# Kernel tuning notes

Measured on AMD Instinct MI355X. Metric: run time of the kernel, lower is better.

The kernel has to match this reference:

```python
import jax, jax.numpy as jnp
import numpy as np
import math

IMG = 224
PATCH = 14
E = 1024          # transformer width (ViT-L/14)
H = 16            # num heads
DH = E // H       # head dim
LAYERS = 24
FF = 4 * E        # CLIP MLP hidden
NROI = 32         # number of ROI bboxes
NSIDE = IMG // PATCH
NPATCH = NSIDE * NSIDE  # 256
T = 1 + NPATCH    # sequence length incl. CLS
INIT = 0.02
EPS_LN = 1e-5


def setup_inputs() -> dict:
    key = jax.random.key(0)
    ks = jax.random.split(key, 16)
    frame = jax.random.uniform(ks[0], (3, IMG, IMG), dtype=jnp.float32)
    # valid bboxes in pixel coords: x1<x2, y1<y2
    c = jax.random.uniform(ks[1], (NROI, 2), dtype=jnp.float32) * (IMG - 40.0) + 20.0
    s = jax.random.uniform(ks[2], (NROI, 2), dtype=jnp.float32) * 60.0 + 20.0
    bboxes = jnp.stack([c[:, 0] - s[:, 0] / 2, c[:, 1] - s[:, 1] / 2,
                        c[:, 0] + s[:, 0] / 2, c[:, 1] + s[:, 1] / 2], axis=-1)
    bboxes = jnp.clip(bboxes, 0.0, float(IMG))
    f32 = jnp.float32
    conv_w = jax.random.normal(ks[3], (E, 3, PATCH, PATCH), f32) * INIT
    cls_emb = jax.random.normal(ks[4], (E,), f32) * INIT
    wq = jax.random.normal(ks[5], (LAYERS, E, E), f32) * INIT
    wk = jax.random.normal(ks[6], (LAYERS, E, E), f32) * INIT
    wv = jax.random.normal(ks[7], (LAYERS, E, E), f32) * INIT
    wo = jax.random.normal(ks[8], (LAYERS, E, E), f32) * INIT
    bq = jnp.zeros((LAYERS, E), f32); bk = jnp.zeros((LAYERS, E), f32)
    bv = jnp.zeros((LAYERS, E), f32); bo = jnp.zeros((LAYERS, E), f32)
    ln1_s = jnp.ones((LAYERS, E), f32); ln1_b = jnp.zeros((LAYERS, E), f32)
    ln2_s = jnp.ones((LAYERS, E), f32); ln2_b = jnp.zeros((LAYERS, E), f32)
    w1 = jax.random.normal(ks[9], (LAYERS, E, FF), f32) * INIT
    b1 = jnp.zeros((LAYERS, FF), f32)
    w2 = jax.random.normal(ks[10], (LAYERS, FF, E), f32) * INIT
    b2 = jnp.zeros((LAYERS, E), f32)
    return {"frame": frame, "bboxes": bboxes, "conv_w": conv_w, "cls_emb": cls_emb,
            "ln1_s": ln1_s, "ln1_b": ln1_b, "wq": wq, "bq": bq, "wk": wk, "bk": bk,
            "wv": wv, "bv": bv, "wo": wo, "bo": bo, "ln2_s": ln2_s, "ln2_b": ln2_b,
            "w1": w1, "b1": b1, "w2": w2, "b2": b2}


def _patch_coords():
    r = jnp.arange(NSIDE, dtype=jnp.float32)
    c = jnp.arange(NSIDE, dtype=jnp.float32)
    cc, rr = jnp.meshgrid(c, r)  # row-major like the python loop
    x1 = (cc * PATCH).reshape(-1); y1 = (rr * PATCH).reshape(-1)
    return jnp.stack([x1, y1, x1 + PATCH, y1 + PATCH], axis=-1)  # (NPATCH,4)


def _overlap_ratio(bboxes, patches):
    # intersection area / patch area -> Mi (N, NPATCH)
    bx1, by1, bx2, by2 = [bboxes[:, None, i] for i in range(4)]
    px1, py1, px2, py2 = [patches[None, :, i] for i in range(4)]
    iw = jnp.clip(jnp.minimum(bx2, px2) - jnp.maximum(bx1, px1), 0.0)
    ih = jnp.clip(jnp.minimum(by2, py2) - jnp.maximum(by1, py1), 0.0)
    parea = (px2 - px1) * (py2 - py1)
    return iw * ih / parea


def _ln(x, s, b):
    m = jnp.mean(x, axis=-1, keepdims=True)
    v = jnp.var(x, axis=-1, keepdims=True)
    return (x - m) * jax.lax.rsqrt(v + EPS_LN) * s + b


def _quick_gelu(x):
    return x * jax.nn.sigmoid(1.702 * x)


def _forward(frame, bboxes, conv_w, cls_emb, ln1_s, ln1_b, wq, bq, wk, bk,
             wv, bv, wo, bo, ln2_s, ln2_b, w1, b1, w2, b2):
    # patch embed: conv stride=PATCH, then relu (as in module forward)
    x = jax.lax.conv_general_dilated(frame[None], conv_w, (PATCH, PATCH), 'VALID',
                                     dimension_numbers=('NCHW', 'OIHW', 'NCHW'))
    x = jax.nn.relu(x)                      # (1, E, NSIDE, NSIDE)
    x = x.reshape(E, NPATCH).T              # (NPATCH, E)
    x = jnp.concatenate([cls_emb[None, :], x], axis=0)  # (T, E)

    Mi = _overlap_ratio(bboxes, _patch_coords())  # (NROI, NPATCH)
    pb = Mi.sum(axis=0)
    pb = pb / (pb.max() + 1e-6)
    attn_bias = jnp.zeros((T, T), jnp.float32).at[0, 1:].set(pb)

    scale = 1.0 / math.sqrt(DH)

    def blk(x, p):
        l1s, l1b, Wq, Bq, Wk, Bk, Wv, Bv, Wo, Bo, l2s, l2b, W1, B1, W2, B2 = p
        h = _ln(x, l1s, l1b)
        q = (h @ Wq + Bq).reshape(T, H, DH)
        k = (h @ Wk + Bk).reshape(T, H, DH)
        v = (h @ Wv + Bv).reshape(T, H, DH)
        scores = jnp.einsum('lhd,shd->hls', q, k) * scale + attn_bias[None]
        a = jax.nn.softmax(scores, axis=-1)
        o = jnp.einsum('hls,shd->lhd', a, v).reshape(T, E) @ Wo + Bo
        x = x + o
        h2 = _ln(x, l2s, l2b)
        m = _quick_gelu(h2 @ W1 + B1) @ W2 + B2
        return x + m, None

    x, _ = jax.lax.scan(blk, x, (ln1_s, ln1_b, wq, bq, wk, bk, wv, bv, wo, bo,
                                 ln2_s, ln2_b, w1, b1, w2, b2))

    cls_out = x[0:1]            # (1, E)
    patch_out = x[1:]           # (NPATCH, E)
    roi = Mi @ patch_out        # (NROI, E)
    return jnp.concatenate([cls_out, roi], axis=0)  # (1+NROI, E)


def reference(frame, bboxes, conv_w, cls_emb, ln1_s, ln1_b, wq, bq, wk, bk,
              wv, bv, wo, bo, ln2_s, ln2_b, w1, b1, w2, b2):
    return _forward(frame, bboxes, conv_w, cls_emb, ln1_s, ln1_b, wq, bq, wk, bk,
                    wv, bv, wo, bo, ln2_s, ln2_b, w1, b1, w2, b2)
```

## Files before the change

kernel.cpp:

```cpp
#include <hip/hip_runtime.h>
#include <hip/hip_bf16.h>
#include <math.h>

#define E_DIM 1024
#define FF_DIM 4096
#define LAYERS 24
#define MPAD 384
#define SPAD 288
#define KCP 608

typedef __attribute__((ext_vector_type(8))) short short8;
typedef __attribute__((ext_vector_type(8))) __bf16 bf16x8;
typedef __attribute__((ext_vector_type(4))) float float4_t;
typedef __attribute__((ext_vector_type(4))) unsigned short ushort4_t;

union ABu { short8 s; bf16x8 b; };
union BFU { __bf16 b; unsigned short u; };

__device__ __forceinline__ float4_t MFMA(bf16x8 a, bf16x8 b, float4_t c) {
  return __builtin_amdgcn_mfma_f32_16x16x32_bf16(a, b, c, 0, 0, 0);
}
__device__ __forceinline__ float4_t MFMAs(short8 a, short8 b, float4_t c) {
  ABu ua, ub; ua.s = a; ub.s = b;
  return __builtin_amdgcn_mfma_f32_16x16x32_bf16(ua.b, ub.b, c, 0, 0, 0);
}
__device__ __forceinline__ unsigned short f2bf(float f) {
  BFU x; x.b = (__bf16)f; return x.u;
}

__device__ __forceinline__ void glds16(const float* src, float* dst) {
  __builtin_amdgcn_global_load_lds(
      (const __attribute__((address_space(1))) unsigned int*)src,
      (__attribute__((address_space(3))) unsigned int*)dst, 16, 0, 0);
}

__global__ void prep_kernel(const float* __restrict__ frame, const float* __restrict__ conv_w,
                            unsigned short* __restrict__ Pm, unsigned short* __restrict__ Wp,
                            unsigned short* __restrict__ h, unsigned short* __restrict__ ob,
                            unsigned short* __restrict__ vTb) {
  int b = blockIdx.x, tid = threadIdx.x;
  if (b < 256) {
    int pr = b >> 4, pc = b & 15;
    for (int kk = tid; kk < KCP; kk += 256) {
      unsigned short us = 0;
      if (kk < 588) {
        int c = kk / 196, rem = kk % 196;
        int i = rem / 14, j = rem % 14;
        us = f2bf(frame[c * 224 * 224 + (pr * 14 + i) * 224 + (pc * 14 + j)]);
      }
      Pm[b * KCP + kk] = us;
    }
  } else if (b < 1280) {
    int n = b - 256;
    for (int kk = tid; kk < KCP; kk += 256) {
      unsigned short us = (kk < 588) ? f2bf(conv_w[n * 588 + kk]) : (unsigned short)0;
      Wp[n * KCP + kk] = us;
    }
  } else {
    int idx = (b - 1280) * 256 + tid;
    const int NH = (MPAD - 257) * E_DIM;
    const int NO = (MPAD - 272) * E_DIM;
    const int NV = 16 * 64 * (SPAD - 272);
    if (idx < NH) {
      h[257 * E_DIM + idx] = 0;
    } else if (idx < NH + NO) {
      ob[272 * E_DIM + (idx - NH)] = 0;
    } else if (idx < NH + NO + NV) {
      int i = idx - NH - NO;
      vTb[(size_t)(i >> 4) * SPAD + 272 + (i & 15)] = 0;
    }
  }
}

__global__ void pb_cls_kernel(const float* __restrict__ bboxes, const float* __restrict__ cls_emb,
                              float* __restrict__ pb, float* __restrict__ Mi, float* __restrict__ x) {
  __shared__ float sb[128];
  __shared__ float red[256];
  int tid = threadIdx.x;
  if (tid < 128) sb[tid] = bboxes[tid];
  __syncthreads();
  int p = tid;
  float px1 = (float)((p & 15) * 14), py1 = (float)((p >> 4) * 14);
  float px2 = px1 + 14.f, py2 = py1 + 14.f;
  float s = 0.f;
  for (int r = 0; r < 32; ++r) {
    float bx1 = sb[r * 4 + 0], by1 = sb[r * 4 + 1], bx2 = sb[r * 4 + 2], by2 = sb[r * 4 + 3];
    float iw = fmaxf(fminf(bx2, px2) - fmaxf(bx1, px1), 0.f);
    float ih = fmaxf(fminf(by2, py2) - fmaxf(by1, py1), 0.f);
    float ov = iw * ih * (1.f / 196.f);
    Mi[r * 256 + p] = ov;
    s += ov;
  }
  red[tid] = s;
  __syncthreads();
  for (int off = 128; off > 0; off >>= 1) {
    if (tid < off) red[tid] = fmaxf(red[tid], red[tid + off]);
    __syncthreads();
  }
  pb[p] = s / (red[0] + 1e-6f);
  for (int j = 0; j < 4; ++j) x[tid * 4 + j] = cls_emb[tid * 4 + j];
}

__global__ __launch_bounds__(256) void conv_gemm(const unsigned short* __restrict__ Pm,
                                                 const unsigned short* __restrict__ Wp,
                                                 float* __restrict__ x) {
  int n0 = blockIdx.x * 16;
  int tid = threadIdx.x, wave = tid >> 6, lane = tid & 63;
  int lg = lane >> 4, lc = lane & 15;
  float4_t acc[4] = {{0,0,0,0},{0,0,0,0},{0,0,0,0},{0,0,0,0}};
  const unsigned short* bp = Wp + (size_t)(n0 + lc) * KCP + lg * 8;
  const unsigned short* apt[4];
#pragma unroll
  for (int t = 0; t < 4; ++t) apt[t] = Pm + (size_t)((wave + t * 4) * 16 + lc) * KCP + lg * 8;
  for (int s = 0; s < 19; ++s) {
    short8 bf = *(const short8*)bp; bp += 32;
#pragma unroll
    for (int t = 0; t < 4; ++t) {
      short8 af = *(const short8*)apt[t]; apt[t] += 32;
      acc[t] = MFMAs(af, bf, acc[t]);
    }
  }
#pragma unroll
  for (int t = 0; t < 4; ++t) {
    int mbase = (wave + t * 4) * 16 + lg * 4;
#pragma unroll
    for (int r = 0; r < 4; ++r)
      x[(size_t)(1 + mbase + r) * E_DIM + n0 + lc] = fmaxf(acc[t][r], 0.f);
  }
}

template <int NTOT, int EPI, int NK>
__global__ __launch_bounds__(256, 1) void gemm_nk(
    const unsigned short* __restrict__ A, int lda,
    const float* __restrict__ Wa, const float* __restrict__ Wb2, const float* __restrict__ Wc,
    const float* __restrict__ ba, const float* __restrict__ bb, const float* __restrict__ bc,
    int NNT,
    unsigned short* __restrict__ oq, unsigned short* __restrict__ okk,
    unsigned short* __restrict__ ovT, unsigned short* __restrict__ om,
    float* __restrict__ opart) {
  static_assert(NK >= 2, "pipeline needs >=2 K-tiles");
  __shared__ __align__(16) float Wt[3][128][32];
  int b = blockIdx.x;
  int p = ((b >> 4) << 3) | (b & 7);
  int mh = (b >> 3) & 1;
  int nt = p % NNT, ks = p / NNT;

  int tid = threadIdx.x, wave = tid >> 6, lane = tid & 63;
  int lg = lane >> 4, lc = lane & 15;

  const float* W; const float* bias; int ncl;
  if (EPI == 0) {
    int sel = nt >> 5; ncl = (nt & 31) << 5;
    W = (sel == 0) ? Wa : ((sel == 1) ? Wb2 : Wc);
    bias = (sel == 0) ? ba : ((sel == 1) ? bb : bc);
  } else {
    ncl = nt << 5; W = Wa; bias = ba;
  }

  const int kb0 = ks * (NK * 128);

  const float* wsrc[4];
  int dsto[4];
#pragma unroll
  for (int op = 0; op < 4; ++op) {
    int rbase = wave * 32 + op * 8;
    int row = rbase + (lane >> 3);
    int key = 8 * ((wave * 4 + op) & 3);
    int col = ((lane & 7) * 4) ^ key;
    wsrc[op] = W + (size_t)(kb0 + row) * NTOT + ncl + col;
    dsto[op] = __builtin_amdgcn_readfirstlane(rbase * 32);
  }

  const unsigned short* ap[3];
#pragma unroll
  for (int j = 0; j < 3; ++j) {
    int t0 = mh * 12 + wave * 3 + j;
    ap[j] = A + (size_t)(t0 * 16 + lc) * lda + kb0 + lg * 8;
  }

  float4_t acc[6];
#pragma unroll
  for (int i = 0; i < 6; ++i) acc[i] = (float4_t){0, 0, 0, 0};

  short8 av[2][12];
#pragma unroll
  for (int s = 0; s < 4; ++s)
#pragma unroll
    for (int j = 0; j < 3; ++j)
      av[0][s * 3 + j] = *(const short8*)(ap[j] + s * 32);
#pragma unroll
  for (int j = 0; j < 3; ++j) ap[j] += 128;

#pragma unroll
  for (int op = 0; op < 4; ++op) glds16(wsrc[op], &Wt[0][0][0] + dsto[op]);
#pragma unroll
  for (int op = 0; op < 4; ++op)
    glds16(wsrc[op] + (size_t)128 * NTOT, &Wt[1][0][0] + dsto[op]);
  asm volatile("s_waitcnt vmcnt(4)\n\ts_barrier" ::: "memory");

  const int cx0 = lg * 256 + (lc ^ (8 * lg));
  const int cx1 = lg * 256 + ((16 + lc) ^ (8 * lg));

#pragma unroll
  for (int t = 0; t < NK; ++t) {
    if (t + 1 < NK) {
#pragma unroll
      for (int s = 0; s < 4; ++s)
#pragma unroll
        for (int j = 0; j < 3; ++j)
          av[(t + 1) & 1][s * 3 + j] = *(const short8*)(ap[j] + s * 32);
#pragma unroll
      for (int j = 0; j < 3; ++j) ap[j] += 128;
    }
    if (t + 2 < NK) {
      float* bufn = &Wt[(t + 2) % 3][0][0];
#pragma unroll
      for (int op = 0; op < 4; ++op)
        glds16(wsrc[op] + (size_t)(t + 2) * 128 * NTOT, bufn + dsto[op]);
    }
    const float* Wb_ = &Wt[t % 3][0][0];
#pragma unroll
    for (int s = 0; s < 4; ++s) {
      bf16x8 wf0, wf1;
#pragma unroll
      for (int d = 0; d < 8; ++d) {
        wf0[d] = (__bf16)Wb_[s * 1024 + cx0 + d * 32];
        wf1[d] = (__bf16)Wb_[s * 1024 + cx1 + d * 32];
      }
#pragma unroll
      for (int j = 0; j < 3; ++j) {
        ABu a; a.s = av[t & 1][s * 3 + j];
        acc[j * 2 + 0] = MFMA(wf0, a.b, acc[j * 2 + 0]);
        acc[j * 2 + 1] = MFMA(wf1, a.b, acc[j * 2 + 1]);
      }
    }
    if (t + 1 < NK) {
      if (t + 2 < NK) asm volatile("s_waitcnt vmcnt(4)\n\ts_barrier" ::: "memory");
      else            asm volatile("s_waitcnt vmcnt(0)\n\ts_barrier" ::: "memory");
    }
  }

  float4_t bv0 = {0,0,0,0}, bv1 = {0,0,0,0};
  if (bias) {
    bv0 = *(const float4_t*)(bias + ncl + lg * 4);
    bv1 = *(const float4_t*)(bias + ncl + 16 + lg * 4);
  }

  if (EPI == 0) {
    int sel = nt >> 5;
    int head = ncl >> 6;
    int db0 = (ncl & 63) + lg * 4;
    int db1 = (ncl & 63) + 16 + lg * 4;
#pragma unroll
    for (int j = 0; j < 3; ++j) {
      int tile = mh * 12 + wave * 3 + j;
      int m = tile * 16 + lc;
      if (sel < 2) {
        unsigned short* dst = (sel == 0 ? oq : okk) + ((size_t)(head * MPAD + m)) * 64;
        ushort4_t h0, h1;
#pragma unroll
        for (int r = 0; r < 4; ++r) {
          h0[r] = f2bf(acc[j * 2 + 0][r] + bv0[r]);
          h1[r] = f2bf(acc[j * 2 + 1][r] + bv1[r]);
        }
        *(ushort4_t*)(dst + db0) = h0;
        *(ushort4_t*)(dst + db1) = h1;
      } else if (tile < 17) {
#pragma unroll
        for (int r = 0; r < 4; ++r) {
          ovT[(size_t)(head * 64 + db0 + r) * SPAD + m] = f2bf(acc[j * 2 + 0][r] + bv0[r]);
          ovT[(size_t)(head * 64 + db1 + r) * SPAD + m] = f2bf(acc[j * 2 + 1][r] + bv1[r]);
        }
      }
    }
  } else if (EPI == 1) {
#pragma unroll
    for (int j = 0; j < 3; ++j) {
      int m = (mh * 12 + wave * 3 + j) * 16 + lc;
      ushort4_t h0, h1;
#pragma unroll
      for (int r = 0; r < 4; ++r) {
        float v0 = acc[j * 2 + 0][r] + bv0[r];
        float v1 = acc[j * 2 + 1][r] + bv1[r];
        h0[r] = f2bf(v0 / (1.f + __expf(-1.702f * v0)));
        h1[r] = f2bf(v1 / (1.f + __expf(-1.702f * v1)));
      }
      *(ushort4_t*)(om + (size_t)m * FF_DIM + ncl + lg * 4) = h0;
      *(ushort4_t*)(om + (size_t)m * FF_DIM + ncl + 16 + lg * 4) = h1;
    }
  } else {
#pragma unroll
    for (int j = 0; j < 3; ++j) {
      int m = (mh * 12 + wave * 3 + j) * 16 + lc;
      float* dst = opart + ((size_t)ks * MPAD + m) * E_DIM + ncl + lg * 4;
      *(float4_t*)dst = acc[j * 2 + 0];
      *(float4_t*)(dst + 16) = acc[j * 2 + 1];
    }
  }
}

__global__ __launch_bounds__(256) void attn_kernel(
    const unsigned short* __restrict__ qb, const unsigned short* __restrict__ kb,
    const unsigned short* __restrict__ vT, const float* __restrict__ pb,
    unsigned short* __restrict__ ob) {
  int head = blockIdx.x / 17, qt = blockIdx.x % 17;
  int q0 = qt * 16;
  int tid = threadIdx.x, wave = tid >> 6, lane = tid & 63;
  int lg = lane >> 4, lc = lane & 15;
  const unsigned short* qh = qb + (size_t)head * MPAD * 64;
  const unsigned short* kh = kb + (size_t)head * MPAD * 64;
  const unsigned short* vh = vT + (size_t)head * 64 * SPAD;

  short8 aq0 = *(const short8*)(qh + (size_t)(q0 + lc) * 64 + lg * 8);
  short8 aq1 = *(const short8*)(qh + (size_t)(q0 + lc) * 64 + 32 + lg * 8);

  float4_t sc[5];
  int st[5]; int nst = 0;
#pragma unroll
  for (int j = 0; j < 5; ++j) {
    int t = wave + j * 4;
    st[j] = (t < 17) ? t : 0;
    if (t < 17) nst = j + 1;
    sc[j] = (float4_t){0,0,0,0};
  }
#pragma unroll
  for (int j = 0; j < 5; ++j) {
    if (j < nst) {
      const unsigned short* kp = kh + (size_t)(st[j] * 16 + lc) * 64 + lg * 8;
      short8 b0 = *(const short8*)kp;
      short8 b1 = *(const short8*)(kp + 32);
      sc[j] = MFMAs(aq0, b0, sc[j]);
      sc[j] = MFMAs(aq1, b1, sc[j]);
    }
  }
  float mx[4] = {-1e30f, -1e30f, -1e30f, -1e30f};
#pragma unroll
  for (int j = 0; j < 5; ++j) {
    if (j < nst) {
      int sg = st[j] * 16 + lc;
#pragma unroll
      for (int r = 0; r < 4; ++r) {
        float v = sc[j][r] * 0.125f;
        if (sg >= 257) v = -1e30f;
        else if (q0 + lg * 4 + r == 0 && sg >= 1) v += pb[sg - 1];
        sc[j][r] = v;
        mx[r] = fmaxf(mx[r], v);
      }
    }
  }
#pragma unroll
  for (int r = 0; r < 4; ++r) {
    mx[r] = fmaxf(mx[r], __shfl_xor(mx[r], 1, 64));
    mx[r] = fmaxf(mx[r], __shfl_xor(mx[r], 2, 64));
    mx[r] = fmaxf(mx[r], __shfl_xor(mx[r], 4, 64));
    mx[r] = fmaxf(mx[r], __shfl_xor(mx[r], 8, 64));
  }
  __shared__ float smax[4][16];
  __shared__ float sden[4][16];
  __shared__ __align__(16) unsigned short P[16][SPAD];
  if (lc == 0) {
#pragma unroll
    for (int r = 0; r < 4; ++r) smax[wave][lg * 4 + r] = mx[r];
  }
  __syncthreads();
  float fm[4], den[4] = {0, 0, 0, 0};
#pragma unroll
  for (int r = 0; r < 4; ++r) {
    int qq = lg * 4 + r;
    fm[r] = fmaxf(fmaxf(smax[0][qq], smax[1][qq]), fmaxf(smax[2][qq], smax[3][qq]));
  }
#pragma unroll
  for (int j = 0; j < 5; ++j) {
    if (j < nst) {
#pragma unroll
      for (int r = 0; r < 4; ++r) {
        float pe = __expf(sc[j][r] - fm[r]);
        sc[j][r] = pe;
        den[r] += pe;
      }
    }
  }
#pragma unroll
  for (int r = 0; r < 4; ++r) {
    den[r] += __shfl_xor(den[r], 1, 64);
    den[r] += __shfl_xor(den[r], 2, 64);
    den[r] += __shfl_xor(den[r], 4, 64);
    den[r] += __shfl_xor(den[r], 8, 64);
  }
  if (lc == 0) {
#pragma unroll
    for (int r = 0; r < 4; ++r) sden[wave][lg * 4 + r] = den[r];
  }
  P[tid >> 4][272 + (tid & 15)] = 0;
#pragma unroll
  for (int j = 0; j < 5; ++j) {
    if (j < nst) {
#pragma unroll
      for (int r = 0; r < 4; ++r) P[lg * 4 + r][st[j] * 16 + lc] = f2bf(sc[j][r]);
    }
  }
  __syncthreads();
  float denf[4];
#pragma unroll
  for (int r = 0; r < 4; ++r) {
    int qq = lg * 4 + r;
    denf[r] = sden[0][qq] + sden[1][qq] + sden[2][qq] + sden[3][qq];
  }
  int d0 = wave * 16;
  float4_t oa = {0, 0, 0, 0};
#pragma unroll
  for (int s9 = 0; s9 < 9; ++s9) {
    short8 pa = *(const short8*)(&P[lc][s9 * 32 + lg * 8]);
    short8 bv = *(const short8*)(vh + (size_t)(d0 + lc) * SPAD + s9 * 32 + lg * 8);
    oa = MFMAs(pa, bv, oa);
  }
#pragma unroll
  for (int r = 0; r < 4; ++r) {
    int qg = q0 + lg * 4 + r;
    ob[(size_t)qg * E_DIM + head * 64 + d0 + lc] = f2bf(oa[r] / denf[r]);
  }
}

__global__ __launch_bounds__(256) void reduce_ln_kernel(
    float* __restrict__ x, const float* __restrict__ part, int nparts,
    const float* __restrict__ rbias,
    const float* __restrict__ lns, const float* __restrict__ lnb,
    unsigned short* __restrict__ hout) {
  int m = blockIdx.x, tid = threadIdx.x;
  int c0 = tid * 4;
  float4_t v = *(const float4_t*)(x + (size_t)m * E_DIM + c0);
  if (rbias) v += *(const float4_t*)(rbias + c0);
  for (int s = 0; s < nparts; ++s)
    v += *(const float4_t*)(part + ((size_t)s * MPAD + m) * E_DIM + c0);
  if (nparts > 0) *(float4_t*)(x + (size_t)m * E_DIM + c0) = v;
  float s1 = v[0] + v[1] + v[2] + v[3];
  float s2 = v[0] * v[0] + v[1] * v[1] + v[2] * v[2] + v[3] * v[3];
#pragma unroll
  for (int off = 1; off < 64; off <<= 1) {
    s1 += __shfl_xor(s1, off, 64);
    s2 += __shfl_xor(s2, off, 64);
  }
  __shared__ float red[8];
  int wave = tid >> 6, lane = tid & 63;
  if (lane == 0) { red[wave * 2] = s1; red[wave * 2 + 1] = s2; }
  __syncthreads();
  s1 = red[0] + red[2] + red[4] + red[6];
  s2 = red[1] + red[3] + red[5] + red[7];
  float mean = s1 * (1.f / 1024.f);
  float var = s2 * (1.f / 1024.f) - mean * mean;
  float rstd = rsqrtf(var + 1e-5f);
  float4_t ls = *(const float4_t*)(lns + c0);
  float4_t lb = *(const float4_t*)(lnb + c0);
  ushort4_t hv;
#pragma unroll
  for (int r = 0; r < 4; ++r) hv[r] = f2bf((v[r] - mean) * rstd * ls[r] + lb[r]);
  *(ushort4_t*)(hout + (size_t)m * E_DIM + c0) = hv;
}

__global__ __launch_bounds__(256) void roi_kernel(const float* __restrict__ x,
                                                  const float* __restrict__ Mi,
                                                  float* __restrict__ out) {
  int b = blockIdx.x, tid = threadIdx.x;
  int c0 = tid * 4;
  if (b == 0) {
    *(float4_t*)(out + c0) = *(const float4_t*)(x + c0);
  } else {
    __shared__ float mi[256];
    mi[tid] = Mi[(b - 1) * 256 + tid];
    __syncthreads();
    float4_t acc = {0, 0, 0, 0};
    for (int p = 0; p < 256; ++p) {
      float4_t xv = *(const float4_t*)(x + (size_t)(1 + p) * E_DIM + c0);
      acc += mi[p] * xv;
    }
    *(float4_t*)(out + (size_t)b * E_DIM + c0) = acc;
  }
}

extern "C" void kernel_launch(void* const* d_in, const int* in_sizes, int n_in,
                              void* d_out, int out_size, void* d_ws, size_t ws_size,
                              hipStream_t stream) {
  const float* frame   = (const float*)d_in[0];
  const float* bboxes  = (const float*)d_in[1];
  const float* conv_w  = (const float*)d_in[2];
  const float* cls_emb = (const float*)d_in[3];
  const float* ln1_s   = (const float*)d_in[4];
  const float* ln1_b   = (const float*)d_in[5];
  const float* wq = (const float*)d_in[6];
  const float* bq = (const float*)d_in[7];
  const float* wk = (const float*)d_in[8];
  const float* bk = (const float*)d_in[9];
  const float* wv = (const float*)d_in[10];
  const float* bv = (const float*)d_in[11];
  const float* wo = (const float*)d_in[12];
  const float* bo = (const float*)d_in[13];
  const float* ln2_s = (const float*)d_in[14];
  const float* ln2_b = (const float*)d_in[15];
  const float* w1 = (const float*)d_in[16];
  const float* b1 = (const float*)d_in[17];
  const float* w2 = (const float*)d_in[18];
  const float* b2 = (const float*)d_in[19];

  char* base = (char*)d_ws;
  auto carve = [&](size_t bytes) {
    char* r = base;
    base += (bytes + 255) & ~(size_t)255;
    return r;
  };
  float* x            = (float*)carve((size_t)257 * E_DIM * 4);
  unsigned short* h   = (unsigned short*)carve((size_t)MPAD * E_DIM * 2);
  unsigned short* qb  = (unsigned short*)carve((size_t)16 * MPAD * 64 * 2);
  unsigned short* kbf = (unsigned short*)carve((size_t)16 * MPAD * 64 * 2);
  unsigned short* vTb = (unsigned short*)carve((size_t)16 * 64 * SPAD * 2);
  unsigned short* ob  = (unsigned short*)carve((size_t)MPAD * E_DIM * 2);
  unsigned short* mb  = (unsigned short*)carve((size_t)MPAD * FF_DIM * 2);
  float* part         = (float*)carve((size_t)4 * MPAD * E_DIM * 4);
  float* pbv          = (float*)carve(256 * 4);
  float* Mi           = (float*)carve(32 * 256 * 4);
  unsigned short* Pm  = (unsigned short*)carve((size_t)256 * KCP * 2);
  unsigned short* Wp  = (unsigned short*)carve((size_t)1024 * KCP * 2);

  prep_kernel<<<1280 + 1020, 256, 0, stream>>>(frame, conv_w, Pm, Wp, h, ob, vTb);
  pb_cls_kernel<<<1, 256, 0, stream>>>(bboxes, cls_emb, pbv, Mi, x);
  conv_gemm<<<64, 256, 0, stream>>>(Pm, Wp, x);
  reduce_ln_kernel<<<257, 256, 0, stream>>>(x, nullptr, 0, nullptr, ln1_s, ln1_b, h);

  for (int l = 0; l < LAYERS; ++l) {
    size_t o2  = (size_t)l * E_DIM * E_DIM;
    size_t o1  = (size_t)l * E_DIM;
    size_t of1 = (size_t)l * E_DIM * FF_DIM;
    size_t ofb = (size_t)l * FF_DIM;
    gemm_nk<1024, 0, 8><<<192, 256, 0, stream>>>(h, E_DIM, wq + o2, wk + o2, wv + o2,
                                                 bq + o1, bk + o1, bv + o1,
                                                 96, qb, kbf, vTb, nullptr, nullptr);
    attn_kernel<<<272, 256, 0, stream>>>(qb, kbf, vTb, pbv, ob);
    gemm_nk<1024, 2, 2><<<256, 256, 0, stream>>>(ob, E_DIM, wo + o2, nullptr, nullptr,
                                                 nullptr, nullptr, nullptr,
                                                 32, nullptr, nullptr, nullptr, nullptr, part);
    reduce_ln_kernel<<<257, 256, 0, stream>>>(x, part, 4, bo + o1, ln2_s + o1, ln2_b + o1, h);
    gemm_nk<4096, 1, 8><<<256, 256, 0, stream>>>(h, E_DIM, w1 + of1, nullptr, nullptr,
                                                 b1 + ofb, nullptr, nullptr,
                                                 128, nullptr, nullptr, nullptr, mb, nullptr);
    gemm_nk<1024, 2, 8><<<256, 256, 0, stream>>>(mb, FF_DIM, w2 + of1, nullptr, nullptr,
                                                 nullptr, nullptr, nullptr,
                                                 32, nullptr, nullptr, nullptr, nullptr, part);
    const float* nls = (l < LAYERS - 1) ? (ln1_s + (size_t)(l + 1) * E_DIM) : ln1_s;
    const float* nlb = (l < LAYERS - 1) ? (ln1_b + (size_t)(l + 1) * E_DIM) : ln1_b;
    reduce_ln_kernel<<<257, 256, 0, stream>>>(x, part, 4, b2 + o1, nls, nlb, h);
  }
  roi_kernel<<<33, 256, 0, stream>>>(x, Mi, (float*)d_out);
}
```

Baseline: 2.042 ms.

## Stage GEMM weights through registers as bf16 in LDS with manual pipeline

After: 1.800 ms. 1.13x faster.

```diff
diff --git a/kernel.cpp b/kernel.cpp
--- a/kernel.cpp
+++ b/kernel.cpp
@@ -17,21 +17,12 @@
 union ABu { short8 s; bf16x8 b; };
 union BFU { __bf16 b; unsigned short u; };
 
-__device__ __forceinline__ float4_t MFMA(bf16x8 a, bf16x8 b, float4_t c) {
-  return __builtin_amdgcn_mfma_f32_16x16x32_bf16(a, b, c, 0, 0, 0);
-}
 __device__ __forceinline__ float4_t MFMAs(short8 a, short8 b, float4_t c) {
   ABu ua, ub; ua.s = a; ub.s = b;
   return __builtin_amdgcn_mfma_f32_16x16x32_bf16(ua.b, ub.b, c, 0, 0, 0);
 }
 __device__ __forceinline__ unsigned short f2bf(float f) {
   BFU x; x.b = (__bf16)f; return x.u;
-}
-
-__device__ __forceinline__ void glds16(const float* src, float* dst) {
-  __builtin_amdgcn_global_load_lds(
-      (const __attribute__((address_space(1))) unsigned int*)src,
-      (__attribute__((address_space(3))) unsigned int*)dst, 16, 0, 0);
 }
 
 __global__ void prep_kernel(const float* __restrict__ frame, const float* __restrict__ conv_w,
@@ -129,6 +120,9 @@
   }
 }
 
+#define WAITB(n) asm volatile("s_waitcnt vmcnt(" #n ") lgkmcnt(0)\n\ts_barrier" ::: "memory")
+#define WAITV(n) asm volatile("s_waitcnt vmcnt(" #n ")" ::: "memory")
+
 template <int NTOT, int EPI, int NK>
 __global__ __launch_bounds__(256, 1) void gemm_nk(
     const unsigned short* __restrict__ A, int lda,
@@ -138,8 +132,8 @@
     unsigned short* __restrict__ oq, unsigned short* __restrict__ okk,
     unsigned short* __restrict__ ovT, unsigned short* __restrict__ om,
     float* __restrict__ opart) {
-  static_assert(NK >= 2, "pipeline needs >=2 K-tiles");
-  __shared__ __align__(16) float Wt[3][128][32];
+  static_assert(NK == 2 || NK >= 3, "NK>=2");
+  __shared__ __align__(16) char WbT[3 * 8192];
   int b = blockIdx.x;
   int p = ((b >> 4) << 3) | (b & 7);
   int mh = (b >> 3) & 1;
@@ -159,17 +153,11 @@
 
   const int kb0 = ks * (NK * 128);
 
-  const float* wsrc[4];
-  int dsto[4];
-#pragma unroll
-  for (int op = 0; op < 4; ++op) {
-    int rbase = wave * 32 + op * 8;
-    int row = rbase + (lane >> 3);
-    int key = 8 * ((wave * 4 + op) & 3);
-    int col = ((lane & 7) * 4) ^ key;
-    wsrc[op] = W + (size_t)(kb0 + row) * NTOT + ncl + col;
-    dsto[op] = __builtin_amdgcn_readfirstlane(rbase * 32);
-  }
+  const int scol = tid & 31, rg = tid >> 5;
+  const int skey = (scol & 7) * 16;
+  const float* gsrc = W + (size_t)(kb0 + rg * 16) * NTOT + ncl + scol;
+  const int wo0 = scol * 256 + ((rg * 32) ^ skey);
+  const int wo1 = scol * 256 + ((rg * 32 + 16) ^ skey);
 
   const unsigned short* ap[3];
 #pragma unroll
@@ -182,63 +170,59 @@
 #pragma unroll
   for (int i = 0; i < 6; ++i) acc[i] = (float4_t){0, 0, 0, 0};
 
+  float g[2][16];
   short8 av[2][12];
-#pragma unroll
-  for (int s = 0; s < 4; ++s)
-#pragma unroll
-    for (int j = 0; j < 3; ++j)
-      av[0][s * 3 + j] = *(const short8*)(ap[j] + s * 32);
-#pragma unroll
-  for (int j = 0; j < 3; ++j) ap[j] += 128;
-
-#pragma unroll
-  for (int op = 0; op < 4; ++op) glds16(wsrc[op], &Wt[0][0][0] + dsto[op]);
-#pragma unroll
-  for (int op = 0; op < 4; ++op)
-    glds16(wsrc[op] + (size_t)128 * NTOT, &Wt[1][0][0] + dsto[op]);
-  asm volatile("s_waitcnt vmcnt(4)\n\ts_barrier" ::: "memory");
-
-  const int cx0 = lg * 256 + (lc ^ (8 * lg));
-  const int cx1 = lg * 256 + ((16 + lc) ^ (8 * lg));
-
-#pragma unroll
-  for (int t = 0; t < NK; ++t) {
-    if (t + 1 < NK) {
-#pragma unroll
-      for (int s = 0; s < 4; ++s)
-#pragma unroll
-        for (int j = 0; j < 3; ++j)
-          av[(t + 1) & 1][s * 3 + j] = *(const short8*)(ap[j] + s * 32);
-#pragma unroll
-      for (int j = 0; j < 3; ++j) ap[j] += 128;
-    }
-    if (t + 2 < NK) {
-      float* bufn = &Wt[(t + 2) % 3][0][0];
-#pragma unroll
-      for (int op = 0; op < 4; ++op)
-        glds16(wsrc[op] + (size_t)(t + 2) * 128 * NTOT, bufn + dsto[op]);
-    }
-    const float* Wb_ = &Wt[t % 3][0][0];
-#pragma unroll
-    for (int s = 0; s < 4; ++s) {
-      bf16x8 wf0, wf1;
-#pragma unroll
-      for (int d = 0; d < 8; ++d) {
-        wf0[d] = (__bf16)Wb_[s * 1024 + cx0 + d * 32];
-        wf1[d] = (__bf16)Wb_[s * 1024 + cx1 + d * 32];
-      }
-#pragma unroll
-      for (int j = 0; j < 3; ++j) {
-        ABu a; a.s = av[t & 1][s * 3 + j];
-        acc[j * 2 + 0] = MFMA(wf0, a.b, acc[j * 2 + 0]);
-        acc[j * 2 + 1] = MFMA(wf1, a.b, acc[j * 2 + 1]);
-      }
-    }
-    if (t + 1 < NK) {
-      if (t + 2 < NK) asm volatile("s_waitcnt vmcnt(4)\n\ts_barrier" ::: "memory");
-      else            asm volatile("s_waitcnt vmcnt(0)\n\ts_barrier" ::: "memory");
-    }
-  }
+  const int keyr = (lc & 7) * 16;
+
+#define ISSUE_G(slot, t) { _Pragma("unroll") for (int j = 0; j < 16; ++j) \
+    g[slot][j] = gsrc[(size_t)(t) * 128 * NTOT + (size_t)j * NTOT]; }
+#define ISSUE_A(slot, t) { _Pragma("unroll") for (int s = 0; s < 4; ++s) \
+    _Pragma("unroll") for (int j = 0; j < 3; ++j) \
+      av[slot][s * 3 + j] = *(const short8*)(ap[j] + (size_t)(t) * 128 + s * 32); }
+#define WRITE_G(slot, t) { short8 wlo, whi; \
+    _Pragma("unroll") for (int j = 0; j < 8; ++j) { \
+      wlo[j] = (short)f2bf(g[slot][j]); whi[j] = (short)f2bf(g[slot][8 + j]); } \
+    char* dstb = WbT + ((t) % 3) * 8192; \
+    *(short8*)(dstb + wo0) = wlo; \
+    *(short8*)(dstb + wo1) = whi; }
+#define COMP(t) { const char* ldsb = WbT + ((t) % 3) * 8192; \
+    _Pragma("unroll") for (int s = 0; s < 4; ++s) { \
+      int o = (s * 64 + lg * 16) ^ keyr; \
+      short8 wf0 = *(const short8*)(ldsb + lc * 256 + o); \
+      short8 wf1 = *(const short8*)(ldsb + (lc + 16) * 256 + o); \
+      _Pragma("unroll") for (int j = 0; j < 3; ++j) { \
+        acc[j * 2 + 0] = MFMAs(wf0, av[(t) & 1][s * 3 + j], acc[j * 2 + 0]); \
+        acc[j * 2 + 1] = MFMAs(wf1, av[(t) & 1][s * 3 + j], acc[j * 2 + 1]); } } }
+
+  if constexpr (NK == 2) {
+    ISSUE_G(0, 0) ISSUE_G(1, 1) ISSUE_A(0, 0) ISSUE_A(1, 1)
+    WAITV(24);
+    WRITE_G(0, 0) WRITE_G(1, 1)
+    asm volatile("s_waitcnt lgkmcnt(0)\n\ts_barrier" ::: "memory");
+    WAITV(12);
+    COMP(0)
+    WAITV(0);
+    COMP(1)
+  } else {
+    ISSUE_G(0, 0) ISSUE_G(1, 1) ISSUE_A(0, 0)
+    WAITV(28);
+    WRITE_G(0, 0)
+    ISSUE_G(0, 2) ISSUE_A(1, 1)
+#pragma unroll
+    for (int t = 0; t < NK; ++t) {
+      if (t <= NK - 3)      { WAITB(28); }
+      else if (t == NK - 2) { WAITB(12); }
+      else                  { WAITB(0);  }
+      if (t + 1 < NK) WRITE_G((t + 1) & 1, t + 1)
+      COMP(t)
+      if (t + 3 < NK) ISSUE_G((t + 3) & 1, t + 3)
+      if (t + 2 < NK) ISSUE_A(t & 1, t + 2)
+    }
+  }
+#undef ISSUE_G
+#undef ISSUE_A
+#undef WRITE_G
+#undef COMP
 
   float4_t bv0 = {0,0,0,0}, bv1 = {0,0,0,0};
   if (bias) {
```
